# Optimization experiments

Hardware: AMD Instinct MI355X
Metric: run time of the kernel (lower is better)

The kernel has to match this reference:

```python
import jax, jax.numpy as jnp
import numpy as np

IN_FEATURES = 1024
N_CLASSES = 50257
CUTOFFS = [0, 5000, 20000, 50257]  # cluster boundaries (lows/highs)


def setup_inputs() -> dict:
    key = jax.random.key(0)
    ks = jax.random.split(key, 6)
    tokens = jax.random.randint(ks[0], (8, 4096), 0, N_CLASSES, dtype=jnp.int32)
    scale = 0.02
    head_emb = jax.random.normal(ks[1], (5000, IN_FEATURES), jnp.float32) * scale
    # tail cluster 0: hsz = 1024 // 2 = 512, osz = 20000 - 5000 = 15000
    tail0_emb = jax.random.normal(ks[2], (15000, 512), jnp.float32) * scale
    tail0_w = jax.random.normal(ks[3], (IN_FEATURES, 512), jnp.float32) * scale  # torch Linear weight (out, in)
    # tail cluster 1: hsz = 1024 // 4 = 256, osz = 50257 - 20000 = 30257
    tail1_emb = jax.random.normal(ks[4], (30257, 256), jnp.float32) * scale
    tail1_w = jax.random.normal(ks[5], (IN_FEATURES, 256), jnp.float32) * scale
    return {"tokens": tokens, "head_emb": head_emb, "tail0_emb": tail0_emb,
            "tail0_w": tail0_w, "tail1_emb": tail1_emb, "tail1_w": tail1_w}


def reference(tokens, head_emb, tail0_emb, tail0_w, tail1_emb, tail1_w):
    # AdaptiveInput forward (eval mode: Dropout = identity).
    # Each token id falls in exactly one cluster [low, high); lookup in that
    # cluster's table (shifted by low), project tails to in_features, scatter
    # back. We express gather+scatter as masked adds (clusters are disjoint).
    B, S = tokens.shape
    t = tokens.reshape(-1)  # [N]

    def cluster_out(low, high, table, w=None):
        mask = ((t >= low) & (t < high))[:, None]                 # [N, 1]
        idx = jnp.clip(t - low, 0, table.shape[0] - 1)            # in-range gather
        e = table[idx]                                            # [N, hsz]
        if w is not None:
            e = e @ w.T                                           # [N, in_features]
        return jnp.where(mask, e, jnp.zeros((), e.dtype))

    out = cluster_out(CUTOFFS[0], CUTOFFS[1], head_emb)
    out = out + cluster_out(CUTOFFS[1], CUTOFFS[2], tail0_emb, tail0_w)
    out = out + cluster_out(CUTOFFS[2], CUTOFFS[3], tail1_emb, tail1_w)
    return out.reshape(B, S, IN_FEATURES)
```

## Files before the change

### kernel.cpp

```cpp
#include <hip/hip_runtime.h>
#include <hip/hip_bf16.h>


typedef __attribute__((ext_vector_type(8))) short short8;
typedef __attribute__((ext_vector_type(4))) float f32x4;

__device__ __forceinline__ unsigned int pk2bf(float a, float b) {
    __hip_bfloat162 h = __float22bfloat162_rn(make_float2(a, b));
    union { __hip_bfloat162 h; unsigned int u; } c; c.h = h; return c.u;
}

__global__ void ai_zero_cnt(int* cnt) {
    if (threadIdx.x < 4) cnt[threadIdx.x] = 0;
}

__global__ __launch_bounds__(256) void ai_partition(const int* __restrict__ tokens, int n,
                             int* __restrict__ cnt,
                             int* __restrict__ l0, int* __restrict__ l1) {
    int i = blockIdx.x * blockDim.x + threadIdx.x;
    if (i >= n) return;
    int lane = threadIdx.x & 63;
    int t = tokens[i];
    int c = (t >= 20000) ? 1 : (t >= 5000) ? 0 : 2;

    unsigned long long act = __ballot(1);
    unsigned long long m0 = __ballot(c == 0);
    unsigned long long m1 = __ballot(c == 1);
    unsigned long long m2 = __ballot(c == 2);
    int leader = __ffsll(act) - 1;

    int b0 = 0, b1 = 0, b2 = 0;
    if (lane == leader) {
        b0 = atomicAdd(&cnt[0], __popcll(m0));
        b1 = atomicAdd(&cnt[1], __popcll(m1));
        b2 = atomicAdd(&cnt[2], __popcll(m2));
    }
    b0 = __shfl(b0, leader);
    b1 = __shfl(b1, leader);
    b2 = __shfl(b2, leader);

    unsigned long long lt = (1ull << lane) - 1ull;
    if (c == 0)      l0[b0 + __popcll(m0 & lt)] = i;
    else if (c == 1) l1[b1 + __popcll(m1 & lt)] = i;
    else             l1[n - 1 - (b2 + __popcll(m2 & lt))] = i;
}

__global__ __launch_bounds__(256) void ai_head_copy(const int* __restrict__ tokens,
                                                    const int* __restrict__ l1, int n,
                                                    const int* __restrict__ cnt,
                                                    const float* __restrict__ emb,
                                                    float* __restrict__ out) {
    const int hc = cnt[2];
    for (int m = blockIdx.x; m < hc; m += gridDim.x) {
        int p = l1[n - 1 - m];
        int t = tokens[p];
        const float4* src = (const float4*)(emb + (size_t)t * 1024);
        float4* dst = (float4*)(out + (size_t)p * 1024);
        dst[threadIdx.x] = src[threadIdx.x];
    }
}

__global__ __launch_bounds__(256) void ai_cvt_w(const float* __restrict__ w0, const float* __restrict__ w1,
                                                unsigned short* __restrict__ o0, unsigned short* __restrict__ o1) {
    int i = blockIdx.x * blockDim.x + threadIdx.x;
    const float* src; unsigned short* dst; int base;
    if (i < 65536) { src = w0; dst = o0; base = i * 8; }
    else           { src = w1; dst = o1; base = (i - 65536) * 8; }
    float4 a = *(const float4*)(src + base);
    float4 b = *(const float4*)(src + base + 4);
    uint4 q = { pk2bf(a.x, a.y), pk2bf(a.z, a.w), pk2bf(b.x, b.y), pk2bf(b.z, b.w) };
    *(uint4*)(dst + base) = q;
}

template<int K, bool PRE>
__global__ __launch_bounds__(256) void ai_tail_gemm(
    const int* __restrict__ tokens,
    const int* __restrict__ list,
    const int* __restrict__ cnt, int cidx, int low,
    const float* __restrict__ emb,
    const float* __restrict__ wf32,
    const unsigned short* __restrict__ wbf,
    float* __restrict__ out)
{
    constexpr int BK  = 64;
    constexpr int LDK = BK + 8;
    __shared__ __align__(16) unsigned short As[128 * LDK];
    __shared__ __align__(16) unsigned short Bs[128 * LDK];
    __shared__ int s_erow[128];
    __shared__ int s_opos[128];

    const int count = cnt[cidx];
    const int m0 = blockIdx.y * 128;
    if (m0 >= count) return;
    const int n0 = blockIdx.x * 128;
    const int tid = threadIdx.x;

    if (tid < 128) {
        int m = m0 + tid;
        if (m < count) {
            int p = list[m];
            s_opos[tid] = p;
            s_erow[tid] = tokens[p] - low;
        } else {
            s_opos[tid] = -1;
            s_erow[tid] = -1;
        }
    }
    __syncthreads();

    f32x4 acc[4][4];
    #pragma unroll
    for (int i = 0; i < 4; i++)
        #pragma unroll
        for (int j = 0; j < 4; j++)
            acc[i][j] = (f32x4){0.f, 0.f, 0.f, 0.f};

    const int lane = tid & 63;
    const int wave = tid >> 6;
    const int wm = (wave >> 1) * 64;
    const int wn = (wave & 1) * 64;
    const int fr = lane & 15;
    const int fk = (lane >> 4) * 8;

    const int srow  = tid >> 1;
    const int shalf = tid & 1;
    const int er = s_erow[srow];

    for (int kt = 0; kt < K; kt += BK) {
        {
            unsigned short* dst = &As[srow * LDK + shalf * 32];
            if (er >= 0) {
                const float4* src = (const float4*)(emb + (size_t)er * K + kt + shalf * 32);
                #pragma unroll
                for (int j = 0; j < 4; j++) {
                    float4 a = src[2*j], b = src[2*j + 1];
                    uint4 q = { pk2bf(a.x, a.y), pk2bf(a.z, a.w), pk2bf(b.x, b.y), pk2bf(b.z, b.w) };
                    *(uint4*)(dst + j*8) = q;
                }
            } else {
                uint4 z = {0u, 0u, 0u, 0u};
                #pragma unroll
                for (int j = 0; j < 4; j++) *(uint4*)(dst + j*8) = z;
            }
        }
        {
            unsigned short* dst = &Bs[srow * LDK + shalf * 32];
            if (PRE) {
                const uint4* src = (const uint4*)(wbf + (size_t)(n0 + srow) * K + kt + shalf * 32);
                #pragma unroll
                for (int j = 0; j < 4; j++) *(uint4*)(dst + j*8) = src[j];
            } else {
                const float4* src = (const float4*)(wf32 + (size_t)(n0 + srow) * K + kt + shalf * 32);
                #pragma unroll
                for (int j = 0; j < 4; j++) {
                    float4 a = src[2*j], b = src[2*j + 1];
                    uint4 q = { pk2bf(a.x, a.y), pk2bf(a.z, a.w), pk2bf(b.x, b.y), pk2bf(b.z, b.w) };
                    *(uint4*)(dst + j*8) = q;
                }
            }
        }
        __syncthreads();

        #pragma unroll
        for (int kk = 0; kk < BK; kk += 32) {
            short8 af[4], bfr[4];
            #pragma unroll
            for (int f = 0; f < 4; f++) {
                af[f]  = *(const short8*)&As[(wm + f*16 + fr) * LDK + kk + fk];
                bfr[f] = *(const short8*)&Bs[(wn + f*16 + fr) * LDK + kk + fk];
            }
            #pragma unroll
            for (int i = 0; i < 4; i++)
                #pragma unroll
                for (int j = 0; j < 4; j++)
                    acc[i][j] = __builtin_amdgcn_mfma_f32_16x16x32_bf16(af[i], bfr[j], acc[i][j], 0, 0, 0);
        }
        __syncthreads();
    }

    const int rbase = (lane >> 4) * 4;
    #pragma unroll
    for (int i = 0; i < 4; i++) {
        #pragma unroll
        for (int r = 0; r < 4; r++) {
            int ml = wm + i * 16 + rbase + r;
            if (m0 + ml < count) {
                float* orow = out + (size_t)s_opos[ml] * 1024 + n0 + wn + fr;
                orow[0]  = acc[i][0][r];
                orow[16] = acc[i][1][r];
                orow[32] = acc[i][2][r];
                orow[48] = acc[i][3][r];
            }
        }
    }
}

extern "C" void kernel_launch(void* const* d_in, const int* in_sizes, int n_in,
                              void* d_out, int out_size, void* d_ws, size_t ws_size,
                              hipStream_t stream) {
    const int*   tokens   = (const int*)d_in[0];
    const float* head_emb = (const float*)d_in[1];
    const float* t0_emb   = (const float*)d_in[2];
    const float* t0_w     = (const float*)d_in[3];
    const float* t1_emb   = (const float*)d_in[4];
    const float* t1_w     = (const float*)d_in[5];
    float* out = (float*)d_out;
    const int N = in_sizes[0];

    int* cnt = (int*)d_ws;
    int* l0  = cnt + 16;
    int* l1  = l0 + N;
    size_t base_need = 64 + (size_t)2 * N * 4;
    size_t wbf_elems = (size_t)1024 * 512 + (size_t)1024 * 256;
    bool pre = ws_size >= base_need + wbf_elems * 2;
    unsigned short* wbf0 = (unsigned short*)((char*)d_ws + base_need);
    unsigned short* wbf1 = wbf0 + (size_t)1024 * 512;

    ai_zero_cnt<<<1, 64, 0, stream>>>(cnt);
    ai_partition<<<(N + 255) / 256, 256, 0, stream>>>(tokens, N, cnt, l0, l1);
    if (pre) ai_cvt_w<<<(65536 + 32768) / 256, 256, 0, stream>>>(t0_w, t1_w, wbf0, wbf1);
    ai_head_copy<<<1024, 256, 0, stream>>>(tokens, l1, N, cnt, head_emb, out);

    dim3 g(8, (N + 127) / 128);
    if (pre) {
        ai_tail_gemm<512, true><<<g, 256, 0, stream>>>(tokens, l0, cnt, 0,  5000, t0_emb, t0_w, wbf0, out);
        ai_tail_gemm<256, true><<<g, 256, 0, stream>>>(tokens, l1, cnt, 1, 20000, t1_emb, t1_w, wbf1, out);
    } else {
        ai_tail_gemm<512, false><<<g, 256, 0, stream>>>(tokens, l0, cnt, 0,  5000, t0_emb, t0_w, wbf0, out);
        ai_tail_gemm<256, false><<<g, 256, 0, stream>>>(tokens, l1, cnt, 1, 20000, t1_emb, t1_w, wbf1, out);
    }
}
```

Measured before the change: 295.1 us.

## Double-buffer tail GEMM with async LDS loads and merge kernel launches

The tail GEMM now double-buffers the weight tile, using global_load_lds direct-to-LDS copies into an XOR-swizzled layout. The embedding tile is prefetched into registers for the next K step while the current step computes. The two tail GEMMs become one launch indexed by blockIdx.z, and counter zeroing is fused into the weight-conversion kernel. Partition switches to per-block atomics through shared memory. Together these aim to hide global load latency, cut launch count and reduce atomic contention, at the cost of more registers, a runtime K (so the loop count is no longer a compile-time constant), and extra LDS.

```diff
diff --git a/kernel.cpp b/kernel.cpp
--- a/kernel.cpp
+++ b/kernel.cpp
@@ -4,45 +4,59 @@
 
 typedef __attribute__((ext_vector_type(8))) short short8;
 typedef __attribute__((ext_vector_type(4))) float f32x4;
-
-__device__ __forceinline__ unsigned int pk2bf(float a, float b) {
+typedef unsigned int u32;
+
+__device__ __forceinline__ u32 pk2bf(float a, float b) {
     __hip_bfloat162 h = __float22bfloat162_rn(make_float2(a, b));
-    union { __hip_bfloat162 h; unsigned int u; } c; c.h = h; return c.u;
-}
-
-__global__ void ai_zero_cnt(int* cnt) {
-    if (threadIdx.x < 4) cnt[threadIdx.x] = 0;
+    union { __hip_bfloat162 h; u32 u; } c; c.h = h; return c.u;
+}
+
+__device__ __forceinline__ void glds16(const void* g, void* l) {
+    __builtin_amdgcn_global_load_lds((const __attribute__((address_space(1))) u32*)g,
+                                     (__attribute__((address_space(3))) u32*)l, 16, 0, 0);
+}
+
+__global__ __launch_bounds__(256) void ai_prep(const float* __restrict__ w0, const float* __restrict__ w1,
+                                               unsigned short* __restrict__ o0, unsigned short* __restrict__ o1,
+                                               int* __restrict__ cnt, int do_cvt) {
+    if (blockIdx.x == 0 && threadIdx.x < 8) cnt[threadIdx.x] = 0;
+    if (!do_cvt) return;
+    int i = blockIdx.x * blockDim.x + threadIdx.x;
+    const float* src; unsigned short* dst; int base;
+    if (i < 65536) { src = w0; dst = o0; base = i * 8; }
+    else           { src = w1; dst = o1; base = (i - 65536) * 8; }
+    float4 a = *(const float4*)(src + base);
+    float4 b = *(const float4*)(src + base + 4);
+    uint4 q = { pk2bf(a.x, a.y), pk2bf(a.z, a.w), pk2bf(b.x, b.y), pk2bf(b.z, b.w) };
+    *(uint4*)(dst + base) = q;
 }
 
 __global__ __launch_bounds__(256) void ai_partition(const int* __restrict__ tokens, int n,
-                             int* __restrict__ cnt,
-                             int* __restrict__ l0, int* __restrict__ l1) {
+                                                    int* __restrict__ cnt,
+                                                    int* __restrict__ l0, int* __restrict__ l1) {
+    __shared__ int wcnt[4][3];
+    __shared__ int wbase[4][3];
     int i = blockIdx.x * blockDim.x + threadIdx.x;
-    if (i >= n) return;
-    int lane = threadIdx.x & 63;
-    int t = tokens[i];
-    int c = (t >= 20000) ? 1 : (t >= 5000) ? 0 : 2;
-
-    unsigned long long act = __ballot(1);
+    int lane = threadIdx.x & 63, w = threadIdx.x >> 6;
+    int t = (i < n) ? tokens[i] : -1;
+    int c = (t < 0) ? 3 : (t >= 20000) ? 1 : (t >= 5000) ? 0 : 2;
     unsigned long long m0 = __ballot(c == 0);
     unsigned long long m1 = __ballot(c == 1);
     unsigned long long m2 = __ballot(c == 2);
-    int leader = __ffsll(act) - 1;
-
-    int b0 = 0, b1 = 0, b2 = 0;
-    if (lane == leader) {
-        b0 = atomicAdd(&cnt[0], __popcll(m0));
-        b1 = atomicAdd(&cnt[1], __popcll(m1));
-        b2 = atomicAdd(&cnt[2], __popcll(m2));
-    }
-    b0 = __shfl(b0, leader);
-    b1 = __shfl(b1, leader);
-    b2 = __shfl(b2, leader);
-
+    if (lane == 0) { wcnt[w][0] = __popcll(m0); wcnt[w][1] = __popcll(m1); wcnt[w][2] = __popcll(m2); }
+    __syncthreads();
+    if (threadIdx.x < 3) {
+        int j = threadIdx.x;
+        int s0 = wcnt[0][j], s1 = wcnt[1][j], s2 = wcnt[2][j], s3 = wcnt[3][j];
+        int base = atomicAdd(&cnt[j], s0 + s1 + s2 + s3);
+        wbase[0][j] = base; wbase[1][j] = base + s0;
+        wbase[2][j] = base + s0 + s1; wbase[3][j] = base + s0 + s1 + s2;
+    }
+    __syncthreads();
     unsigned long long lt = (1ull << lane) - 1ull;
-    if (c == 0)      l0[b0 + __popcll(m0 & lt)] = i;
-    else if (c == 1) l1[b1 + __popcll(m1 & lt)] = i;
-    else             l1[n - 1 - (b2 + __popcll(m2 & lt))] = i;
+    if (c == 0)      l0[wbase[w][0] + __popcll(m0 & lt)] = i;
+    else if (c == 1) l1[wbase[w][1] + __popcll(m1 & lt)] = i;
+    else if (c == 2) l1[n - 1 - (wbase[w][2] + __popcll(m2 & lt))] = i;
 }
 
 __global__ __launch_bounds__(256) void ai_head_copy(const int* __restrict__ tokens,
@@ -60,36 +74,32 @@
     }
 }
 
-__global__ __launch_bounds__(256) void ai_cvt_w(const float* __restrict__ w0, const float* __restrict__ w1,
-                                                unsigned short* __restrict__ o0, unsigned short* __restrict__ o1) {
-    int i = blockIdx.x * blockDim.x + threadIdx.x;
-    const float* src; unsigned short* dst; int base;
-    if (i < 65536) { src = w0; dst = o0; base = i * 8; }
-    else           { src = w1; dst = o1; base = (i - 65536) * 8; }
-    float4 a = *(const float4*)(src + base);
-    float4 b = *(const float4*)(src + base + 4);
-    uint4 q = { pk2bf(a.x, a.y), pk2bf(a.z, a.w), pk2bf(b.x, b.y), pk2bf(b.z, b.w) };
-    *(uint4*)(dst + base) = q;
-}
-
-template<int K, bool PRE>
+template<bool PRE>
 __global__ __launch_bounds__(256) void ai_tail_gemm(
     const int* __restrict__ tokens,
-    const int* __restrict__ list,
-    const int* __restrict__ cnt, int cidx, int low,
-    const float* __restrict__ emb,
-    const float* __restrict__ wf32,
-    const unsigned short* __restrict__ wbf,
+    const int* __restrict__ l0, const int* __restrict__ l1,
+    const int* __restrict__ cnt,
+    const float* __restrict__ emb0, const float* __restrict__ emb1,
+    const float* __restrict__ w0f, const float* __restrict__ w1f,
+    const unsigned short* __restrict__ w0b, const unsigned short* __restrict__ w1b,
     float* __restrict__ out)
 {
-    constexpr int BK  = 64;
-    constexpr int LDK = BK + 8;
-    __shared__ __align__(16) unsigned short As[128 * LDK];
-    __shared__ __align__(16) unsigned short Bs[128 * LDK];
+    constexpr int BK = 64;
+    constexpr int LDKA = 72;
+    __shared__ __align__(16) unsigned short As[128 * LDKA];
+    __shared__ __align__(16) unsigned short Bs[2][128 * BK];
     __shared__ int s_erow[128];
     __shared__ int s_opos[128];
 
-    const int count = cnt[cidx];
+    const int z = blockIdx.z;
+    const int K     = z ? 256 : 512;
+    const int low   = z ? 20000 : 5000;
+    const int count = cnt[z];
+    const int* list = z ? l1 : l0;
+    const float* emb = z ? emb1 : emb0;
+    const float* wf  = z ? w1f : w0f;
+    const unsigned short* wb = z ? w1b : w0b;
+
     const int m0 = blockIdx.y * 128;
     if (m0 >= count) return;
     const int n0 = blockIdx.x * 128;
@@ -121,61 +131,107 @@
     const int wn = (wave & 1) * 64;
     const int fr = lane & 15;
     const int fk = (lane >> 4) * 8;
+    const int swzm = (fr & 7) << 4;
 
     const int srow  = tid >> 1;
     const int shalf = tid & 1;
     const int er = s_erow[srow];
 
-    for (int kt = 0; kt < K; kt += BK) {
-        {
-            unsigned short* dst = &As[srow * LDK + shalf * 32];
-            if (er >= 0) {
-                const float4* src = (const float4*)(emb + (size_t)er * K + kt + shalf * 32);
-                #pragma unroll
-                for (int j = 0; j < 4; j++) {
-                    float4 a = src[2*j], b = src[2*j + 1];
-                    uint4 q = { pk2bf(a.x, a.y), pk2bf(a.z, a.w), pk2bf(b.x, b.y), pk2bf(b.z, b.w) };
-                    *(uint4*)(dst + j*8) = q;
-                }
-            } else {
-                uint4 z = {0u, 0u, 0u, 0u};
-                #pragma unroll
-                for (int j = 0; j < 4; j++) *(uint4*)(dst + j*8) = z;
-            }
-        }
-        {
-            unsigned short* dst = &Bs[srow * LDK + shalf * 32];
-            if (PRE) {
-                const uint4* src = (const uint4*)(wbf + (size_t)(n0 + srow) * K + kt + shalf * 32);
-                #pragma unroll
-                for (int j = 0; j < 4; j++) *(uint4*)(dst + j*8) = src[j];
-            } else {
-                const float4* src = (const float4*)(wf32 + (size_t)(n0 + srow) * K + kt + shalf * 32);
-                #pragma unroll
-                for (int j = 0; j < 4; j++) {
-                    float4 a = src[2*j], b = src[2*j + 1];
-                    uint4 q = { pk2bf(a.x, a.y), pk2bf(a.z, a.w), pk2bf(b.x, b.y), pk2bf(b.z, b.w) };
-                    *(uint4*)(dst + j*8) = q;
-                }
-            }
-        }
-        __syncthreads();
-
+    const int rlc  = lane >> 3;
+    const int c16s = (lane & 7) ^ rlc;
+
+    float4 areg[8];
+    float4 breg[8];
+
+    auto loadA = [&](int kt) {
+        if (er >= 0) {
+            const float4* src = (const float4*)(emb + (size_t)er * K + kt + shalf * 32);
+            #pragma unroll
+            for (int j = 0; j < 8; j++) areg[j] = src[j];
+        }
+    };
+    auto writeA = [&]() {
+        unsigned short* dst = &As[srow * LDKA + shalf * 32];
+        if (er >= 0) {
+            #pragma unroll
+            for (int j = 0; j < 4; j++) {
+                uint4 q = { pk2bf(areg[2*j].x, areg[2*j].y), pk2bf(areg[2*j].z, areg[2*j].w),
+                            pk2bf(areg[2*j+1].x, areg[2*j+1].y), pk2bf(areg[2*j+1].z, areg[2*j+1].w) };
+                *(uint4*)(dst + j * 8) = q;
+            }
+        } else {
+            uint4 zq = {0u, 0u, 0u, 0u};
+            #pragma unroll
+            for (int j = 0; j < 4; j++) *(uint4*)(dst + j * 8) = zq;
+        }
+    };
+    auto issueB = [&](int kt, int buf) {
+        if (PRE) {
+            #pragma unroll
+            for (int i = 0; i < 4; i++) {
+                int chunk = wave * 4 + i;
+                const unsigned short* src = wb + (size_t)(n0 + chunk * 8 + rlc) * K + kt + c16s * 8;
+                glds16(src, &Bs[buf][chunk * 512]);
+            }
+        } else {
+            const float4* src = (const float4*)(wf + (size_t)(n0 + srow) * K + kt + shalf * 32);
+            #pragma unroll
+            for (int j = 0; j < 8; j++) breg[j] = src[j];
+        }
+    };
+    auto writeB = [&](int buf) {
+        if (!PRE) {
+            char* base = (char*)&Bs[buf][0] + srow * 128;
+            int sm = (srow & 7) << 4;
+            #pragma unroll
+            for (int j = 0; j < 4; j++) {
+                uint4 q = { pk2bf(breg[2*j].x, breg[2*j].y), pk2bf(breg[2*j].z, breg[2*j].w),
+                            pk2bf(breg[2*j+1].x, breg[2*j+1].y), pk2bf(breg[2*j+1].z, breg[2*j+1].w) };
+                *(uint4*)(base + ((shalf * 64 + j * 16) ^ sm)) = q;
+            }
+        }
+    };
+
+    auto compute = [&](int buf) {
+        const char* Bbase = (const char*)&Bs[buf][0];
         #pragma unroll
         for (int kk = 0; kk < BK; kk += 32) {
-            short8 af[4], bfr[4];
+            short8 af[4], bf[4];
             #pragma unroll
             for (int f = 0; f < 4; f++) {
-                af[f]  = *(const short8*)&As[(wm + f*16 + fr) * LDK + kk + fk];
-                bfr[f] = *(const short8*)&Bs[(wn + f*16 + fr) * LDK + kk + fk];
+                af[f] = *(const short8*)&As[(wm + f * 16 + fr) * LDKA + kk + fk];
+                int rb = wn + f * 16 + fr;
+                bf[f] = *(const short8*)(Bbase + rb * 128 + (((kk + fk) << 1) ^ swzm));
             }
             #pragma unroll
             for (int i = 0; i < 4; i++)
                 #pragma unroll
                 for (int j = 0; j < 4; j++)
-                    acc[i][j] = __builtin_amdgcn_mfma_f32_16x16x32_bf16(af[i], bfr[j], acc[i][j], 0, 0, 0);
-        }
+                    acc[i][j] = __builtin_amdgcn_mfma_f32_16x16x32_bf16(af[i], bf[j], acc[i][j], 0, 0, 0);
+        }
+    };
+
+    issueB(0, 0);
+    loadA(0);
+    writeA();
+    writeB(0);
+    __syncthreads();
+
+    const int nt = K / BK;
+    for (int t = 0; t < nt; t++) {
+        const int cur = t & 1;
+        const bool more = (t + 1 < nt);
+        if (more) {
+            issueB((t + 1) * BK, cur ^ 1);
+            loadA((t + 1) * BK);
+        }
+        compute(cur);
         __syncthreads();
+        if (more) {
+            writeA();
+            writeB(cur ^ 1);
+            __syncthreads();
+        }
     }
 
     const int rbase = (lane >> 4) * 4;
@@ -216,17 +272,15 @@
     unsigned short* wbf0 = (unsigned short*)((char*)d_ws + base_need);
     unsigned short* wbf1 = wbf0 + (size_t)1024 * 512;
 
-    ai_zero_cnt<<<1, 64, 0, stream>>>(cnt);
+    ai_prep<<<384, 256, 0, stream>>>(t0_w, t1_w, wbf0, wbf1, cnt, pre ? 1 : 0);
     ai_partition<<<(N + 255) / 256, 256, 0, stream>>>(tokens, N, cnt, l0, l1);
-    if (pre) ai_cvt_w<<<(65536 + 32768) / 256, 256, 0, stream>>>(t0_w, t1_w, wbf0, wbf1);
     ai_head_copy<<<1024, 256, 0, stream>>>(tokens, l1, N, cnt, head_emb, out);
 
-    dim3 g(8, (N + 127) / 128);
-    if (pre) {
-        ai_tail_gemm<512, true><<<g, 256, 0, stream>>>(tokens, l0, cnt, 0,  5000, t0_emb, t0_w, wbf0, out);
-        ai_tail_gemm<256, true><<<g, 256, 0, stream>>>(tokens, l1, cnt, 1, 20000, t1_emb, t1_w, wbf1, out);
-    } else {
-        ai_tail_gemm<512, false><<<g, 256, 0, stream>>>(tokens, l0, cnt, 0,  5000, t0_emb, t0_w, wbf0, out);
-        ai_tail_gemm<256, false><<<g, 256, 0, stream>>>(tokens, l1, cnt, 1, 20000, t1_emb, t1_w, wbf1, out);
-    }
-}
+    dim3 g(8, (N + 127) / 128, 2);
+    if (pre)
+        ai_tail_gemm<true><<<g, 256, 0, stream>>>(tokens, l0, l1, cnt, t0_emb, t1_emb,
+                                                  t0_w, t1_w, wbf0, wbf1, out);
+    else
+        ai_tail_gemm<false><<<g, 256, 0, stream>>>(tokens, l0, l1, cnt, t0_emb, t1_emb,
+                                                   t0_w, t1_w, wbf0, wbf1, out);
+}
```

Result: faster. 268.9 us (-8.9%).
